# Optimization experiments

Hardware: AMD Instinct MI355X
Metric: run time of the kernel (lower is better)

The kernel has to match this reference:

```python
import jax, jax.numpy as jnp
import numpy as np

LN_EPS = 1e-5
N_NODES, N_EDGES, D_IN, D_HID, N_LAYERS = 50000, 800000, 512, 512, 3


def setup_inputs() -> dict:
    key = jax.random.key(0)
    k0, k1, k2 = jax.random.split(key, 3)
    x = jax.random.normal(k0, (N_NODES, D_IN), dtype=jnp.float32)
    edge_index = jax.random.randint(k1, (2, N_EDGES), 0, N_NODES, dtype=jnp.int32)
    # Glorot-ish scale so activations stay sane through the stack
    Ws = jax.random.normal(k2, (N_LAYERS, D_HID, D_HID), dtype=jnp.float32) / np.float32(np.sqrt(D_HID))
    bs = jnp.zeros((N_LAYERS, D_HID), dtype=jnp.float32)
    gammas = jnp.ones((N_LAYERS, D_HID), dtype=jnp.float32)
    betas = jnp.zeros((N_LAYERS, D_HID), dtype=jnp.float32)
    return {"x": x, "edge_index": edge_index, "Ws": Ws, "bs": bs, "gammas": gammas, "betas": betas}


def _layer_norm(v, gamma, beta):
    mu = jnp.mean(v, axis=-1, keepdims=True)
    vc = v - mu
    var = jnp.mean(vc * vc, axis=-1, keepdims=True)
    return gamma * vc * jax.lax.rsqrt(var + LN_EPS) + beta


def reference(x, edge_index, Ws, bs, gammas, betas):
    src, dst = edge_index[0], edge_index[1]
    n = x.shape[0]
    # GCN degrees with self-loops (graph is fixed across layers)
    deg = 1.0 + jax.ops.segment_sum(jnp.ones(src.shape[0], x.dtype), dst, num_segments=n)
    inv_sqrt = jax.lax.rsqrt(deg)
    enorm = (inv_sqrt[src] * inv_sqrt[dst])[:, None]  # [E,1] symmetric norm
    h = x
    for l in range(Ws.shape[0]):
        ht = h @ Ws[l] + bs[l]                               # [N, D] linear
        agg = jax.ops.segment_sum(ht[src] * enorm, dst, num_segments=n)
        agg = agg + ht / deg[:, None]                        # self-loop term
        # dropout is identity in eval mode; then LayerNorm -> ReLU
        h = jnp.maximum(_layer_norm(agg, gammas[l], betas[l]), 0.0)
    return h
```

## Files before the change

kernel.cpp:

```cpp
#include <hip/hip_runtime.h>

#define N_NODES 50000
#define N_EDGES 800000
#define D_FEAT 512
#define N_LAYERS 3
#define LN_EPS 1e-5f
#define M_PAD 50176
#define N_SBLK ((N_NODES + 255) / 256)
#define BUCK_STRIDE 64
#define BUCK_CAP ((size_t)N_NODES * BUCK_STRIDE + 72)

typedef __attribute__((ext_vector_type(8))) _Float16 half8;
typedef __attribute__((ext_vector_type(4))) _Float16 half4;
typedef __attribute__((ext_vector_type(4))) float f32x4;

__device__ __forceinline__ void gl_lds16(const unsigned short* g, unsigned short* l) {
  __builtin_amdgcn_global_load_lds((const __attribute__((address_space(1))) unsigned int*)g,
                                   (__attribute__((address_space(3))) unsigned int*)l, 16, 0, 0);
}


__global__ __launch_bounds__(256) void count_deg_kernel(const int* __restrict__ ei,
                                                        int* __restrict__ cnt) {
  int e = blockIdx.x * 256 + threadIdx.x;
  if (e < N_EDGES) atomicAdd(&cnt[ei[N_EDGES + e]], 1);
}

__global__ __launch_bounds__(256) void inv_sqrt_kernel(const int* __restrict__ cnt,
                                                       float* __restrict__ inv_sqrt) {
  int i = blockIdx.x * 256 + threadIdx.x;
  if (i < N_NODES) inv_sqrt[i] = rsqrtf(1.0f + (float)cnt[i]);
}

__global__ __launch_bounds__(256) void fill_bucket_kernel(const int* __restrict__ ei,
                                                          int* __restrict__ cursor,
                                                          int2* __restrict__ bucket,
                                                          const float* __restrict__ inv_sqrt) {
  int e = blockIdx.x * 256 + threadIdx.x;
  if (e < N_EDGES) {
    int s = ei[e];
    int d = ei[N_EDGES + e];
    int p = atomicAdd(&cursor[d], 1) & (BUCK_STRIDE - 1);
    int2 pk;
    pk.x = s;
    pk.y = __float_as_int(inv_sqrt[s] * inv_sqrt[d]);
    bucket[(size_t)d * BUCK_STRIDE + p] = pk;
  }
}

__global__ __launch_bounds__(256) void wconv_kernel(const float* __restrict__ Ws,
                                                    _Float16* __restrict__ Bth) {
  __shared__ float t[64][65];
  const float* W = Ws + (size_t)blockIdx.z * D_FEAT * D_FEAT;
  _Float16* Bh = Bth + (size_t)blockIdx.z * D_FEAT * D_FEAT;
  int n0 = blockIdx.x * 64, k0 = blockIdx.y * 64;
  int tid = threadIdx.x;
  int c = tid & 63, r4 = tid >> 6;
#pragma unroll
  for (int r = 0; r < 64; r += 4)
    t[r4 + r][c] = W[(size_t)(k0 + r4 + r) * D_FEAT + n0 + c];
  __syncthreads();
#pragma unroll
  for (int r = 0; r < 64; r += 4) {
    float v = t[c][r4 + r];
    Bh[(size_t)(n0 + r4 + r) * D_FEAT + k0 + c] = (_Float16)v;
  }
}


template <bool FP32A, bool SPLIT>
__global__ __launch_bounds__(256, 3) void mfma_gemm_kernel(
    const _Float16* __restrict__ Ah, const float* __restrict__ Xf,
    const _Float16* __restrict__ Bh, const float* __restrict__ bias,
    _Float16* __restrict__ ht) {
  __shared__ unsigned short sAh[128 * 32];
  __shared__ unsigned short sAl[SPLIT ? 128 * 32 : 8];
  __shared__ unsigned short sBh[128 * 32];

  int tid = threadIdx.x;
  int wave = tid >> 6, lane = tid & 63;

  int id = blockIdx.y * 4 + blockIdx.x;
  int mrow = (id & 7) + 8 * (id >> 5);
  int ncol = (id >> 3) & 3;
  int n0 = ncol * 128, m0 = mrow * 128;

  int r0 = (wave * 2 + 0) * 16 + (lane >> 2);
  int r1 = (wave * 2 + 1) * 16 + (lane >> 2);
  int s0 = (lane & 3) ^ ((r0 >> 1) & 3);
  int s1 = (lane & 3) ^ ((r1 >> 1) & 3);
  size_t gA0 = (size_t)(m0 + r0) * D_FEAT + s0 * 8;
  size_t gA1 = (size_t)(m0 + r1) * D_FEAT + s1 * 8;
  size_t gB0 = (size_t)(n0 + r0) * D_FEAT + s0 * 8;
  size_t gB1 = (size_t)(n0 + r1) * D_FEAT + s1 * 8;
  int l0 = (wave * 2 + 0) * 512;
  int l1 = (wave * 2 + 1) * 512;

  size_t gX0 = 0, gX1 = 0;
  if (FP32A) {
    int rr0 = (m0 + r0 < N_NODES) ? (m0 + r0) : (N_NODES - 1);
    int rr1 = (m0 + r1 < N_NODES) ? (m0 + r1) : (N_NODES - 1);
    gX0 = (size_t)rr0 * D_FEAT + s0 * 8;
    gX1 = (size_t)rr1 * D_FEAT + s1 * 8;
  }

  int q = lane >> 4, fr = lane & 15;
  int wm = (wave >> 1) * 64, wn = (wave & 1) * 64;
  int aoff[4], boff[4];
#pragma unroll
  for (int i = 0; i < 4; ++i) {
    int row = wm + i * 16 + fr;
    aoff[i] = row * 32 + (q ^ ((row >> 1) & 3)) * 8;
  }
#pragma unroll
  for (int j = 0; j < 4; ++j) {
    int row = wn + j * 16 + fr;
    boff[j] = row * 32 + (q ^ ((row >> 1) & 3)) * 8;
  }

  f32x4 acc[4][4];
#pragma unroll
  for (int i = 0; i < 4; ++i)
#pragma unroll
    for (int j = 0; j < 4; ++j) acc[i][j] = (f32x4)0.0f;

  for (int k0 = 0; k0 < D_FEAT; k0 += 32) {
    if constexpr (FP32A) {
      const float* p0 = Xf + gX0 + k0;
      const float* p1 = Xf + gX1 + k0;
      float4 a0 = *(const float4*)p0, b0 = *(const float4*)(p0 + 4);
      float4 a1 = *(const float4*)p1, b1 = *(const float4*)(p1 + 4);
      float f0[8] = {a0.x, a0.y, a0.z, a0.w, b0.x, b0.y, b0.z, b0.w};
      float f1[8] = {a1.x, a1.y, a1.z, a1.w, b1.x, b1.y, b1.z, b1.w};
      half8 h0, lo0, h1, lo1;
#pragma unroll
      for (int k = 0; k < 8; ++k) {
        _Float16 t0 = (_Float16)f0[k]; h0[k] = t0; lo0[k] = (_Float16)(f0[k] - (float)t0);
        _Float16 t1 = (_Float16)f1[k]; h1[k] = t1; lo1[k] = (_Float16)(f1[k] - (float)t1);
      }
      *(half8*)(sAh + l0 + lane * 8) = h0;
      *(half8*)(sAl + l0 + lane * 8) = lo0;
      *(half8*)(sAh + l1 + lane * 8) = h1;
      *(half8*)(sAl + l1 + lane * 8) = lo1;
    } else {
      gl_lds16((const unsigned short*)(Ah + gA0 + k0), sAh + l0);
      gl_lds16((const unsigned short*)(Ah + gA1 + k0), sAh + l1);
    }
    gl_lds16((const unsigned short*)(Bh + gB0 + k0), sBh + l0);
    gl_lds16((const unsigned short*)(Bh + gB1 + k0), sBh + l1);
    __syncthreads();

    half8 ah[4], bh[4];
#pragma unroll
    for (int i = 0; i < 4; ++i) ah[i] = *(const half8*)(sAh + aoff[i]);
#pragma unroll
    for (int j = 0; j < 4; ++j) bh[j] = *(const half8*)(sBh + boff[j]);
#pragma unroll
    for (int i = 0; i < 4; ++i)
#pragma unroll
      for (int j = 0; j < 4; ++j)
        acc[i][j] = __builtin_amdgcn_mfma_f32_16x16x32_f16(ah[i], bh[j], acc[i][j], 0, 0, 0);
    if constexpr (SPLIT) {
      half8 al[4];
#pragma unroll
      for (int i = 0; i < 4; ++i) al[i] = *(const half8*)(sAl + aoff[i]);
#pragma unroll
      for (int i = 0; i < 4; ++i)
#pragma unroll
        for (int j = 0; j < 4; ++j)
          acc[i][j] = __builtin_amdgcn_mfma_f32_16x16x32_f16(al[i], bh[j], acc[i][j], 0, 0, 0);
    }
    __syncthreads();
  }

  float bj[4];
#pragma unroll
  for (int j = 0; j < 4; ++j) bj[j] = bias[n0 + wn + j * 16 + fr];
#pragma unroll
  for (int i = 0; i < 4; ++i) {
    int gm0 = m0 + wm + i * 16 + q * 4;
#pragma unroll
    for (int j = 0; j < 4; ++j) {
      int gn = n0 + wn + j * 16 + fr;
#pragma unroll
      for (int r = 0; r < 4; ++r) {
        int gm = gm0 + r;
        if (gm < N_NODES)
          ht[(size_t)gm * D_FEAT + gn] = (_Float16)(acc[i][j][r] + bj[j]);
      }
    }
  }
}


template <bool LAST>
__global__ __launch_bounds__(256) void agg_ln_relu_kernel(
    const _Float16* __restrict__ ht, const int* __restrict__ deg,
    const int2* __restrict__ bucket, const float* __restrict__ inv_sqrt,
    const float* __restrict__ gamma, const float* __restrict__ beta,
    float* __restrict__ hout, _Float16* __restrict__ ph) {
  int n = blockIdx.x * 4 + (threadIdx.x >> 6);
  int lane = threadIdx.x & 63;
  int c8 = lane * 8;

  half8 vself = *(const half8*)(ht + (size_t)n * D_FEAT + c8);
  float isn = inv_sqrt[n];
  int d = deg[n];

  int ng = (d + 7) >> 3;
  const int2* cp = bucket + (size_t)n * BUCK_STRIDE;

  float acc[8];
#pragma unroll
  for (int k = 0; k < 8; ++k) acc[k] = 0.f;

  if (ng > 0) {
    int2 p[8];
#pragma unroll
    for (int k = 0; k < 8; ++k) p[k] = cp[k];
    for (int g = 0; g < ng; ++g) {
      int lim = d - g * 8;
      int sx[8];
      float w[8];
#pragma unroll
      for (int k = 0; k < 8; ++k) {
        sx[k] = (k < lim) ? p[k].x : n;
        w[k] = (k < lim) ? __int_as_float(p[k].y) : 0.f;
      }
      half8 v[8];
#pragma unroll
      for (int k = 0; k < 8; ++k)
        v[k] = *(const half8*)(ht + (size_t)sx[k] * D_FEAT + c8);
#pragma unroll
      for (int k = 0; k < 8; ++k) p[k] = cp[(g + 1) * 8 + k];
#pragma unroll
      for (int k = 0; k < 8; ++k)
#pragma unroll
        for (int j = 0; j < 8; ++j) acc[j] = fmaf(w[k], (float)v[k][j], acc[j]);
    }
  }
  {
    float w = isn * isn;
#pragma unroll
    for (int k = 0; k < 8; ++k) acc[k] = fmaf(w, (float)vself[k], acc[k]);
  }

  float s = 0.f, s2 = 0.f;
#pragma unroll
  for (int k = 0; k < 8; ++k) { s += acc[k]; s2 += acc[k] * acc[k]; }
#pragma unroll
  for (int off = 32; off > 0; off >>= 1) {
    s += __shfl_xor(s, off);
    s2 += __shfl_xor(s2, off);
  }

  const float inv_d = 1.0f / (float)D_FEAT;
  float mu = s * inv_d;
  float var = s2 * inv_d - mu * mu;
  float rstd = rsqrtf(var + LN_EPS);

  float4 g0 = *(const float4*)(gamma + c8);
  float4 g1 = *(const float4*)(gamma + c8 + 4);
  float4 b0 = *(const float4*)(beta + c8);
  float4 b1 = *(const float4*)(beta + c8 + 4);
  float gg[8] = {g0.x, g0.y, g0.z, g0.w, g1.x, g1.y, g1.z, g1.w};
  float bb[8] = {b0.x, b0.y, b0.z, b0.w, b1.x, b1.y, b1.z, b1.w};

  float o[8];
#pragma unroll
  for (int k = 0; k < 8; ++k)
    o[k] = fmaxf(gg[k] * (acc[k] - mu) * rstd + bb[k], 0.f);

  if (LAST) {
    *(float4*)(hout + (size_t)n * D_FEAT + c8) = make_float4(o[0], o[1], o[2], o[3]);
    *(float4*)(hout + (size_t)n * D_FEAT + c8 + 4) = make_float4(o[4], o[5], o[6], o[7]);
  } else {
    half8 h;
#pragma unroll
    for (int k = 0; k < 8; ++k) h[k] = (_Float16)o[k];
    *(half8*)(ph + (size_t)n * D_FEAT + c8) = h;
  }
}


extern "C" void kernel_launch(void* const* d_in, const int* in_sizes, int n_in,
                              void* d_out, int out_size, void* d_ws, size_t ws_size,
                              hipStream_t stream) {
  const float* x      = (const float*)d_in[0];
  const int*   ei     = (const int*)d_in[1];
  const float* Ws     = (const float*)d_in[2];
  const float* bs     = (const float*)d_in[3];
  const float* gammas = (const float*)d_in[4];
  const float* betas  = (const float*)d_in[5];
  float* out = (float*)d_out;

  _Float16* Ah  = (_Float16*)d_ws;
  _Float16* Bth = Ah + (size_t)M_PAD * D_FEAT;
  _Float16* htb = Bth + (size_t)N_LAYERS * D_FEAT * D_FEAT;
  int2* bucket  = (int2*)(htb + (size_t)N_NODES * D_FEAT);
  float* inv_sqrt = (float*)(bucket + BUCK_CAP);
  int* deg_cnt = (int*)(inv_sqrt + N_NODES);
  int* cursor  = deg_cnt + N_NODES;

  hipMemsetAsync(deg_cnt, 0, N_NODES * sizeof(int), stream);
  hipMemsetAsync(cursor, 0, N_NODES * sizeof(int), stream);
  hipMemsetAsync(Ah + (size_t)N_NODES * D_FEAT, 0,
                 (size_t)(M_PAD - N_NODES) * D_FEAT * sizeof(_Float16), stream);

  count_deg_kernel<<<(N_EDGES + 255) / 256, 256, 0, stream>>>(ei, deg_cnt);
  inv_sqrt_kernel<<<N_SBLK, 256, 0, stream>>>(deg_cnt, inv_sqrt);
  fill_bucket_kernel<<<(N_EDGES + 255) / 256, 256, 0, stream>>>(ei, cursor, bucket, inv_sqrt);

  wconv_kernel<<<dim3(8, 8, N_LAYERS), 256, 0, stream>>>(Ws, Bth);

  dim3 ggrid(D_FEAT / 128, M_PAD / 128);
  for (int l = 0; l < N_LAYERS; ++l) {
    if (l == 0) {
      mfma_gemm_kernel<true, true><<<ggrid, 256, 0, stream>>>(Ah, x, Bth, bs, htb);
    } else {
      mfma_gemm_kernel<false, false><<<ggrid, 256, 0, stream>>>(
          Ah, x, Bth + (size_t)l * D_FEAT * D_FEAT, bs + (size_t)l * D_FEAT, htb);
    }
    if (l < N_LAYERS - 1) {
      agg_ln_relu_kernel<false><<<N_NODES / 4, 256, 0, stream>>>(
          htb, deg_cnt, bucket, inv_sqrt, gammas + (size_t)l * D_FEAT,
          betas + (size_t)l * D_FEAT, nullptr, Ah);
    } else {
      agg_ln_relu_kernel<true><<<N_NODES / 4, 256, 0, stream>>>(
          htb, deg_cnt, bucket, inv_sqrt, gammas + (size_t)l * D_FEAT,
          betas + (size_t)l * D_FEAT, out, nullptr);
    }
  }
}
```

Baseline: 762.8 us.

## Merge degree counting into bucket fill, factor edge norm, drop split-fp16 GEMM

Degree counting now happens inside the bucket-fill pass, because the cursor atomic gives the count, so one edge kernel and one memset go away. The bucket stores only source indices. The aggregation factors the symmetric norm: each neighbour is weighted by inv_sqrt[src], and the destination's inv_sqrt is applied once at the end. This halves bucket traffic but adds a gathered inv_sqrt load per edge. The first-layer GEMM also drops its hi/lo fp16 split of the fp32 input, which halves MFMA work for that layer at the cost of precision on x.

```diff
diff --git a/kernel.cpp b/kernel.cpp
--- a/kernel.cpp
+++ b/kernel.cpp
@@ -20,32 +20,22 @@
 }
 
 
-__global__ __launch_bounds__(256) void count_deg_kernel(const int* __restrict__ ei,
-                                                        int* __restrict__ cnt) {
-  int e = blockIdx.x * 256 + threadIdx.x;
-  if (e < N_EDGES) atomicAdd(&cnt[ei[N_EDGES + e]], 1);
-}
-
-__global__ __launch_bounds__(256) void inv_sqrt_kernel(const int* __restrict__ cnt,
-                                                       float* __restrict__ inv_sqrt) {
-  int i = blockIdx.x * 256 + threadIdx.x;
-  if (i < N_NODES) inv_sqrt[i] = rsqrtf(1.0f + (float)cnt[i]);
-}
-
 __global__ __launch_bounds__(256) void fill_bucket_kernel(const int* __restrict__ ei,
                                                           int* __restrict__ cursor,
-                                                          int2* __restrict__ bucket,
-                                                          const float* __restrict__ inv_sqrt) {
+                                                          int* __restrict__ bucket) {
   int e = blockIdx.x * 256 + threadIdx.x;
   if (e < N_EDGES) {
     int s = ei[e];
     int d = ei[N_EDGES + e];
     int p = atomicAdd(&cursor[d], 1) & (BUCK_STRIDE - 1);
-    int2 pk;
-    pk.x = s;
-    pk.y = __float_as_int(inv_sqrt[s] * inv_sqrt[d]);
-    bucket[(size_t)d * BUCK_STRIDE + p] = pk;
-  }
+    bucket[(size_t)d * BUCK_STRIDE + p] = s;
+  }
+}
+
+__global__ __launch_bounds__(256) void inv_sqrt_kernel(const int* __restrict__ deg,
+                                                       float* __restrict__ inv_sqrt) {
+  int i = blockIdx.x * 256 + threadIdx.x;
+  if (i < N_NODES) inv_sqrt[i] = rsqrtf(1.0f + (float)deg[i]);
 }
 
 __global__ __launch_bounds__(256) void wconv_kernel(const float* __restrict__ Ws,
@@ -68,13 +58,12 @@
 }
 
 
-template <bool FP32A, bool SPLIT>
+template <bool FP32A>
 __global__ __launch_bounds__(256, 3) void mfma_gemm_kernel(
     const _Float16* __restrict__ Ah, const float* __restrict__ Xf,
     const _Float16* __restrict__ Bh, const float* __restrict__ bias,
     _Float16* __restrict__ ht) {
   __shared__ unsigned short sAh[128 * 32];
-  __shared__ unsigned short sAl[SPLIT ? 128 * 32 : 8];
   __shared__ unsigned short sBh[128 * 32];
 
   int tid = threadIdx.x;
@@ -132,16 +121,14 @@
       float4 a1 = *(const float4*)p1, b1 = *(const float4*)(p1 + 4);
       float f0[8] = {a0.x, a0.y, a0.z, a0.w, b0.x, b0.y, b0.z, b0.w};
       float f1[8] = {a1.x, a1.y, a1.z, a1.w, b1.x, b1.y, b1.z, b1.w};
-      half8 h0, lo0, h1, lo1;
+      half8 h0, h1;
 #pragma unroll
       for (int k = 0; k < 8; ++k) {
-        _Float16 t0 = (_Float16)f0[k]; h0[k] = t0; lo0[k] = (_Float16)(f0[k] - (float)t0);
-        _Float16 t1 = (_Float16)f1[k]; h1[k] = t1; lo1[k] = (_Float16)(f1[k] - (float)t1);
+        h0[k] = (_Float16)f0[k];
+        h1[k] = (_Float16)f1[k];
       }
       *(half8*)(sAh + l0 + lane * 8) = h0;
-      *(half8*)(sAl + l0 + lane * 8) = lo0;
       *(half8*)(sAh + l1 + lane * 8) = h1;
-      *(half8*)(sAl + l1 + lane * 8) = lo1;
     } else {
       gl_lds16((const unsigned short*)(Ah + gA0 + k0), sAh + l0);
       gl_lds16((const unsigned short*)(Ah + gA1 + k0), sAh + l1);
@@ -160,16 +147,6 @@
 #pragma unroll
       for (int j = 0; j < 4; ++j)
         acc[i][j] = __builtin_amdgcn_mfma_f32_16x16x32_f16(ah[i], bh[j], acc[i][j], 0, 0, 0);
-    if constexpr (SPLIT) {
-      half8 al[4];
-#pragma unroll
-      for (int i = 0; i < 4; ++i) al[i] = *(const half8*)(sAl + aoff[i]);
-#pragma unroll
-      for (int i = 0; i < 4; ++i)
-#pragma unroll
-        for (int j = 0; j < 4; ++j)
-          acc[i][j] = __builtin_amdgcn_mfma_f32_16x16x32_f16(al[i], bh[j], acc[i][j], 0, 0, 0);
-    }
     __syncthreads();
   }
 
@@ -196,7 +173,7 @@
 template <bool LAST>
 __global__ __launch_bounds__(256) void agg_ln_relu_kernel(
     const _Float16* __restrict__ ht, const int* __restrict__ deg,
-    const int2* __restrict__ bucket, const float* __restrict__ inv_sqrt,
+    const int* __restrict__ bucket, const float* __restrict__ inv_sqrt,
     const float* __restrict__ gamma, const float* __restrict__ beta,
     float* __restrict__ hout, _Float16* __restrict__ ph) {
   int n = blockIdx.x * 4 + (threadIdx.x >> 6);
@@ -208,42 +185,39 @@
   int d = deg[n];
 
   int ng = (d + 7) >> 3;
-  const int2* cp = bucket + (size_t)n * BUCK_STRIDE;
+  const int* cp = bucket + (size_t)n * BUCK_STRIDE;
 
   float acc[8];
 #pragma unroll
   for (int k = 0; k < 8; ++k) acc[k] = 0.f;
 
   if (ng > 0) {
-    int2 p[8];
+    int p[8];
 #pragma unroll
     for (int k = 0; k < 8; ++k) p[k] = cp[k];
     for (int g = 0; g < ng; ++g) {
       int lim = d - g * 8;
       int sx[8];
+#pragma unroll
+      for (int k = 0; k < 8; ++k) sx[k] = (k < lim) ? p[k] : n;
+      half8 v[8];
       float w[8];
 #pragma unroll
       for (int k = 0; k < 8; ++k) {
-        sx[k] = (k < lim) ? p[k].x : n;
-        w[k] = (k < lim) ? __int_as_float(p[k].y) : 0.f;
+        v[k] = *(const half8*)(ht + (size_t)sx[k] * D_FEAT + c8);
+        float ws = inv_sqrt[sx[k]];
+        w[k] = (k < lim) ? ws : 0.f;
       }
-      half8 v[8];
+#pragma unroll
+      for (int k = 0; k < 8; ++k) p[k] = cp[(g + 1) * 8 + k];
 #pragma unroll
       for (int k = 0; k < 8; ++k)
-        v[k] = *(const half8*)(ht + (size_t)sx[k] * D_FEAT + c8);
-#pragma unroll
-      for (int k = 0; k < 8; ++k) p[k] = cp[(g + 1) * 8 + k];
-#pragma unroll
-      for (int k = 0; k < 8; ++k)
 #pragma unroll
         for (int j = 0; j < 8; ++j) acc[j] = fmaf(w[k], (float)v[k][j], acc[j]);
     }
   }
-  {
-    float w = isn * isn;
-#pragma unroll
-    for (int k = 0; k < 8; ++k) acc[k] = fmaf(w, (float)vself[k], acc[k]);
-  }
+#pragma unroll
+  for (int k = 0; k < 8; ++k) acc[k] = isn * fmaf(isn, (float)vself[k], acc[k]);
 
   float s = 0.f, s2 = 0.f;
 #pragma unroll
@@ -297,37 +271,34 @@
   _Float16* Ah  = (_Float16*)d_ws;
   _Float16* Bth = Ah + (size_t)M_PAD * D_FEAT;
   _Float16* htb = Bth + (size_t)N_LAYERS * D_FEAT * D_FEAT;
-  int2* bucket  = (int2*)(htb + (size_t)N_NODES * D_FEAT);
+  int* bucket   = (int*)(htb + (size_t)N_NODES * D_FEAT);
   float* inv_sqrt = (float*)(bucket + BUCK_CAP);
-  int* deg_cnt = (int*)(inv_sqrt + N_NODES);
-  int* cursor  = deg_cnt + N_NODES;
-
-  hipMemsetAsync(deg_cnt, 0, N_NODES * sizeof(int), stream);
-  hipMemsetAsync(cursor, 0, N_NODES * sizeof(int), stream);
+  int* deg_cur  = (int*)(inv_sqrt + N_NODES);
+
+  hipMemsetAsync(deg_cur, 0, N_NODES * sizeof(int), stream);
   hipMemsetAsync(Ah + (size_t)N_NODES * D_FEAT, 0,
                  (size_t)(M_PAD - N_NODES) * D_FEAT * sizeof(_Float16), stream);
 
-  count_deg_kernel<<<(N_EDGES + 255) / 256, 256, 0, stream>>>(ei, deg_cnt);
-  inv_sqrt_kernel<<<N_SBLK, 256, 0, stream>>>(deg_cnt, inv_sqrt);
-  fill_bucket_kernel<<<(N_EDGES + 255) / 256, 256, 0, stream>>>(ei, cursor, bucket, inv_sqrt);
+  fill_bucket_kernel<<<(N_EDGES + 255) / 256, 256, 0, stream>>>(ei, deg_cur, bucket);
+  inv_sqrt_kernel<<<N_SBLK, 256, 0, stream>>>(deg_cur, inv_sqrt);
 
   wconv_kernel<<<dim3(8, 8, N_LAYERS), 256, 0, stream>>>(Ws, Bth);
 
   dim3 ggrid(D_FEAT / 128, M_PAD / 128);
   for (int l = 0; l < N_LAYERS; ++l) {
     if (l == 0) {
-      mfma_gemm_kernel<true, true><<<ggrid, 256, 0, stream>>>(Ah, x, Bth, bs, htb);
+      mfma_gemm_kernel<true><<<ggrid, 256, 0, stream>>>(Ah, x, Bth, bs, htb);
     } else {
-      mfma_gemm_kernel<false, false><<<ggrid, 256, 0, stream>>>(
+      mfma_gemm_kernel<false><<<ggrid, 256, 0, stream>>>(
           Ah, x, Bth + (size_t)l * D_FEAT * D_FEAT, bs + (size_t)l * D_FEAT, htb);
     }
     if (l < N_LAYERS - 1) {
       agg_ln_relu_kernel<false><<<N_NODES / 4, 256, 0, stream>>>(
-          htb, deg_cnt, bucket, inv_sqrt, gammas + (size_t)l * D_FEAT,
+          htb, deg_cur, bucket, inv_sqrt, gammas + (size_t)l * D_FEAT,
           betas + (size_t)l * D_FEAT, nullptr, Ah);
     } else {
       agg_ln_relu_kernel<true><<<N_NODES / 4, 256, 0, stream>>>(
-          htb, deg_cnt, bucket, inv_sqrt, gammas + (size_t)l * D_FEAT,
+          htb, deg_cur, bucket, inv_sqrt, gammas + (size_t)l * D_FEAT,
           betas + (size_t)l * D_FEAT, out, nullptr);
     }
   }
```

Result: faster. 726.8 us (-4.7%).
